# Performance work log

Hardware: AMD Instinct MI355X
Metric: run time of the kernel (lower is better)

The kernel has to match this reference:

```python
import jax, jax.numpy as jnp
import numpy as np

EPS = 1e-5  # torch BatchNorm1d default eps


def setup_inputs() -> dict:
    key = jax.random.key(0)
    ks = jax.random.split(key, 8)
    F, P = 32, 64            # frames, peds per frame
    B = F * P                # batch = 2048
    E, H, M, D = 64, 128, 512, 1024  # embed, h_dim, pool_mlp_dim, bottleneck
    starts = np.arange(F, dtype=np.int64) * P
    seq_start_end = jnp.asarray(np.stack([starts, starts + P], axis=1))
    inp = {
        "curr_h_states": jax.random.normal(ks[0], (1, B, H), dtype=jnp.float32),
        "curr_pos": jax.random.normal(ks[1], (B, 2), dtype=jnp.float32),
        "seq_start_end": seq_start_end,
        # embedding: Linear(2, E)
        "We": jax.random.normal(ks[2], (2, E), dtype=jnp.float32) * 0.5,
        "be": jnp.zeros((E,), dtype=jnp.float32),
        # mlp layer 1: Linear(E+H, M) + BN(M)
        "W1": jax.random.normal(ks[3], (E + H, M), dtype=jnp.float32) * 0.05,
        "b1": jnp.zeros((M,), dtype=jnp.float32),
        "g1": jnp.ones((M,), dtype=jnp.float32),
        "beta1": jnp.zeros((M,), dtype=jnp.float32),
        # mlp layer 2: Linear(M, D) + BN(D)
        "W2": jax.random.normal(ks[4], (M, D), dtype=jnp.float32) * 0.04,
        "b2": jnp.zeros((D,), dtype=jnp.float32),
        "g2": jnp.ones((D,), dtype=jnp.float32),
        "beta2": jnp.zeros((D,), dtype=jnp.float32),
        # BN running stats (eval mode)
        "rm1": jnp.zeros((M,), dtype=jnp.float32),
        "rv1": jnp.ones((M,), dtype=jnp.float32),
        "rm2": jnp.zeros((D,), dtype=jnp.float32),
        "rv2": jnp.ones((D,), dtype=jnp.float32),
    }
    return inp


def _bn(x, g, beta, rm, rv):
    return g * (x - rm) * jax.lax.rsqrt(rv + EPS) + beta


def reference(curr_h_states, curr_pos, seq_start_end, We, be, W1, b1, g1, beta1,
              W2, b2, g2, beta2, rm1, rv1, rm2, rv2):
    # Equal-size frames: vectorize the per-frame Python loop via a reshape.
    F = seq_start_end.shape[0]
    B = curr_h_states.shape[1]
    P = B // F
    h = curr_h_states[0].reshape(F, P, -1)      # (F, P, H)
    pos = curr_pos.reshape(F, P, 2)             # (F, P, 2)
    # rel_pos[f, i, j] = pos[f, j] - pos[f, i]  (repeat minus repeat_interleave)
    rel = pos[:, None, :, :] - pos[:, :, None, :]          # (F, P, P, 2)
    emb = rel @ We + be                                     # (F, P, P, E)
    h_rep = jnp.broadcast_to(h[:, None, :, :], (F, P, P, h.shape[-1]))
    x = jnp.concatenate([emb, h_rep], axis=-1)              # (F, P, P, E+H)
    x = jax.nn.relu(_bn(x @ W1 + b1, g1, beta1, rm1, rv1))  # (F, P, P, M)
    x = jax.nn.relu(_bn(x @ W2 + b2, g2, beta2, rm2, rv2))  # (F, P, P, D)
    pool_h = x.max(axis=2)                                  # max over j -> (F, P, D)
    return pool_h.reshape(B, -1)                            # (B, D)
```

## Files before the change

kernel.cpp:

```cpp
#include <hip/hip_runtime.h>
#include <hip/hip_fp16.h>
#include <stdint.h>

#define EPS_BN 1e-5f

constexpr int Fn = 32;
constexpr int Pn = 64;
constexpr int Bn = 2048;
constexpr int Hn = 128;
constexpr int En = 64;
constexpr int Mn = 512;
constexpr int Dn = 1024;

using f16x8   = __attribute__((ext_vector_type(8))) _Float16;
using f32x16  = __attribute__((ext_vector_type(16))) float;

static __device__ __forceinline__ unsigned short hfbits(float f) {
  return __builtin_bit_cast(unsigned short, __float2half(f));
}

static __device__ __forceinline__ void dma16(const uint4* g, const uint4* l) {
  __builtin_amdgcn_global_load_lds(
      (const __attribute__((address_space(1))) unsigned int*)g,
      (__attribute__((address_space(3))) unsigned int*)l, 16, 0, 0);
}

static __device__ __forceinline__ uint32_t pkmax(uint32_t a, uint32_t b) {
  uint32_t r;
  asm("v_pk_max_f16 %0, %1, %2" : "=v"(r) : "v"(a), "v"(b));
  return r;
}

static __device__ __forceinline__ void mk2(uint4 a0, uint4 a1, uint4 q,
                                           f16x8& r0, f16x8& r1) {
  uint4 x0, x1;
#pragma unroll
  for (int v = 0; v < 4; ++v) {
    uint32_t qw = ((const uint32_t*)&q)[v];
    ((uint32_t*)&x0)[v] = pkmax(((const uint32_t*)&a0)[v], qw);
    ((uint32_t*)&x1)[v] = pkmax(((const uint32_t*)&a1)[v], qw);
  }
  r0 = __builtin_bit_cast(f16x8, x0);
  r1 = __builtin_bit_cast(f16x8, x1);
}

__global__ void prep_all(const float* __restrict__ hs, const float* __restrict__ pos,
                         const float* __restrict__ We, const float* __restrict__ be,
                         const float* __restrict__ W1, const float* __restrict__ b1,
                         const float* __restrict__ g1, const float* __restrict__ beta1,
                         const float* __restrict__ rm1, const float* __restrict__ rv1,
                         const float* __restrict__ W2, const float* __restrict__ b2,
                         const float* __restrict__ g2, const float* __restrict__ beta2,
                         const float* __restrict__ rm2, const float* __restrict__ rv2,
                         __half* __restrict__ Agb, __half* __restrict__ Qgb,
                         uint4* __restrict__ W2g, float* __restrict__ G0,
                         float* __restrict__ G1, float* __restrict__ c2) {
  __shared__ float smem[64 * 65];
  int bid = blockIdx.x, t = threadIdx.x;
  if (bid < 512) {
    int rb = bid * 4, m = t;
    float w0 = 0.f, w1 = 0.f, c = 0.f;
    for (int e = 0; e < En; ++e) {
      float w = W1[e * Mn + m];
      w0 += We[e] * w; w1 += We[En + e] * w; c += be[e] * w;
    }
    c += b1[m];
    float s  = g1[m] * rsqrtf(rv1[m] + EPS_BN);
    float tt = beta1[m] - rm1[m] * s;
    float acc[4];
#pragma unroll
    for (int ri = 0; ri < 4; ++ri) acc[ri] = c;
#pragma unroll 4
    for (int e = 0; e < Hn; ++e) {
      float w = W1[(En + e) * Mn + m];
#pragma unroll
      for (int ri = 0; ri < 4; ++ri)
        acc[ri] += hs[(rb + ri) * Hn + e] * w;
    }
#pragma unroll
    for (int ri = 0; ri < 4; ++ri) {
      float q = pos[(rb + ri) * 2] * w0 + pos[(rb + ri) * 2 + 1] * w1;
      Agb[(rb + ri) * Mn + m] = __float2half((acc[ri] + q) * s + tt);
      Qgb[(rb + ri) * Mn + m] = __float2half(q * s);
    }
  } else if (bid < 640) {
    int b2i = bid - 512;
    int d0 = (b2i & 15) * 64, k0 = (b2i >> 4) * 64;
    int col = t & 63, row8 = t >> 6;
#pragma unroll
    for (int rr = 0; rr < 8; ++rr) {
      int row = rr * 8 + row8;
      smem[row * 65 + col] = W2[(k0 + row) * Dn + d0 + col];
    }
    __syncthreads();
    int lane = t & 63, q8 = t >> 6;
    int sel_n = q8 & 1, sel_ks = q8 >> 1;
    int dl = sel_n * 32 + (lane & 31), d = d0 + dl;
    float sf = g2[d] * rsqrtf(rv2[d] + EPS_BN);
    int kb = sel_ks * 16 + (lane >> 5) * 8;
    uint32_t wd[4];
#pragma unroll
    for (int h = 0; h < 4; ++h) {
      uint32_t u0 = hfbits(smem[(kb + 2 * h) * 65 + dl] * sf);
      uint32_t u1 = hfbits(smem[(kb + 2 * h + 1) * 65 + dl] * sf);
      wd[h] = u0 | (u1 << 16);
    }
    int n32 = (d0 >> 5) + sel_n;
    int ks  = (k0 >> 4) + sel_ks;
    W2g[(n32 * 32 + ks) * 64 + lane] = (uint4){wd[0], wd[1], wd[2], wd[3]};
  } else {
    int gb = bid - 640;
    int d0g = gb * 64;
    float* wr0 = smem;
    float* wr1 = smem + 512;
    {
      int m = t;
      float w0 = 0.f, w1 = 0.f;
      for (int e = 0; e < En; ++e) {
        float w = W1[e * Mn + m];
        w0 += We[e] * w; w1 += We[En + e] * w;
      }
      float s = g1[m] * rsqrtf(rv1[m] + EPS_BN);
      wr0[m] = w0 * s; wr1[m] = w1 * s;
    }
    __syncthreads();
    int dl = t & 63, part = t >> 6;
    float p0 = 0.f, p1 = 0.f;
#pragma unroll 4
    for (int mm = 0; mm < 64; ++mm) {
      int m = part * 64 + mm;
      float wv = W2[m * Dn + d0g + dl];
      p0 += wr0[m] * wv; p1 += wr1[m] * wv;
    }
    float* pr = smem + 1024;
    pr[part * 64 + dl] = p0;
    pr[512 + part * 64 + dl] = p1;
    __syncthreads();
    if (t < 128) {
      int which = t >> 6, dd = d0g + (t & 63);
      float s2v = g2[dd] * rsqrtf(rv2[dd] + EPS_BN);
      float sum = 0.f;
#pragma unroll
      for (int pp = 0; pp < 8; ++pp) sum += pr[which * 512 + pp * 64 + (t & 63)];
      (which ? G1 : G0)[dd] = sum * s2v;
      if (which == 0) c2[dd] = b2[dd] * s2v + beta2[dd] - rm2[dd] * s2v;
    }
  }
}

__launch_bounds__(256, 2)
__global__ void gemm_pool(const __half* __restrict__ Agb,
                          const __half* __restrict__ Qgb,
                          const uint4* __restrict__ W2g,
                          const float* __restrict__ pos,
                          const float* __restrict__ G0, const float* __restrict__ G1,
                          const float* __restrict__ c2, float* __restrict__ out) {
  __shared__ uint4 SH[3328];

  int wg  = blockIdx.x;
  int swz = (wg & 7) * 512 + (wg >> 3);
  int ct  = swz & 7;
  int rt  = swz >> 3;
  int f = rt >> 4, i0 = (rt & 15) * 4;

  int t = threadIdx.x, lane = t & 63, w = t >> 6;
  int i = i0 + w;

  const uint4* aGL = (const uint4*)(Agb + (size_t)f * Pn * Mn) +
                     (size_t)(lane & 31) * 64 + (lane >> 5);
  const uint4* bGL = W2g + (size_t)(4 * ct) * 32 * 64 + lane;

  auto stageAB = [&](int p) {
    int buf = p & 1;
    dma16(aGL + (size_t)0 * 2048 + (p * 4 + w) * 2, SH + buf * 512 + (w * 2 + 0) * 64);
    dma16(aGL + (size_t)1 * 2048 + (p * 4 + w) * 2, SH + buf * 512 + (w * 2 + 1) * 64);
#pragma unroll
    for (int nf = 0; nf < 4; ++nf)
      dma16(bGL + (nf * 32 + p * 4 + w) * 64,
            SH + 1024 + buf * 1024 + (w * 4 + nf) * 64);
  };

  dma16((const uint4*)(Qgb + (size_t)(f * Pn + i) * Mn) + lane, SH + 3072 + w * 64);
  stageAB(0);

  f32x16 acc[2][4];
#pragma unroll
  for (int jf = 0; jf < 2; ++jf)
#pragma unroll
    for (int nf = 0; nf < 4; ++nf)
      acc[jf][nf] = (f32x16){0.f,0.f,0.f,0.f,0.f,0.f,0.f,0.f,
                             0.f,0.f,0.f,0.f,0.f,0.f,0.f,0.f};

  int qb = 3072 + w * 64 + (lane >> 5);

#pragma unroll 1
  for (int p = 0; p < 8; ++p) {
    __syncthreads();
    if (p < 7) stageAB(p + 1);
    int ab = (p & 1) * 512 + lane;
    int bb = 1024 + (p & 1) * 1024 + lane;

#pragma unroll
    for (int ksl = 0; ksl < 4; ++ksl) {
      int ks = p * 4 + ksl;
      uint4 a0 = SH[ab + (ksl * 2 + 0) * 64];
      uint4 a1 = SH[ab + (ksl * 2 + 1) * 64];
      uint4 q  = SH[qb + ks * 2];
      f16x8 af0, af1;
      mk2(a0, a1, q, af0, af1);
#pragma unroll
      for (int nf = 0; nf < 4; ++nf) {
        f16x8 bg = __builtin_bit_cast(f16x8, SH[bb + (ksl * 4 + nf) * 64]);
        acc[0][nf] = __builtin_amdgcn_mfma_f32_32x32x16_f16(af0, bg, acc[0][nf], 0, 0, 0);
        acc[1][nf] = __builtin_amdgcn_mfma_f32_32x32x16_f16(af1, bg, acc[1][nf], 0, 0, 0);
      }
    }
  }

  float px = pos[(f * Pn + i) * 2], py = pos[(f * Pn + i) * 2 + 1];
#pragma unroll
  for (int nf = 0; nf < 4; ++nf) {
    float mx = -3.0e38f;
#pragma unroll
    for (int jf = 0; jf < 2; ++jf)
#pragma unroll
      for (int rg = 0; rg < 16; ++rg)
        mx = fmaxf(mx, acc[jf][nf][rg]);
    mx = fmaxf(mx, __shfl_xor(mx, 32));
    if (lane < 32) {
      int d = ct * 128 + nf * 32 + (lane & 31);
      float r = px * G0[d] + py * G1[d];
      out[(f * Pn + i) * Dn + d] = fmaxf(mx - r + c2[d], 0.f);
    }
  }
}

extern "C" void kernel_launch(void* const* d_in, const int* in_sizes, int n_in,
                              void* d_out, int out_size, void* d_ws, size_t ws_size,
                              hipStream_t stream) {
  const float* hs    = (const float*)d_in[0];
  const float* pos   = (const float*)d_in[1];
  const float* We    = (const float*)d_in[3];
  const float* be    = (const float*)d_in[4];
  const float* W1    = (const float*)d_in[5];
  const float* b1    = (const float*)d_in[6];
  const float* g1    = (const float*)d_in[7];
  const float* beta1 = (const float*)d_in[8];
  const float* W2    = (const float*)d_in[9];
  const float* b2    = (const float*)d_in[10];
  const float* g2    = (const float*)d_in[11];
  const float* beta2 = (const float*)d_in[12];
  const float* rm1   = (const float*)d_in[13];
  const float* rv1   = (const float*)d_in[14];
  const float* rm2   = (const float*)d_in[15];
  const float* rv2   = (const float*)d_in[16];

  char* ws = (char*)d_ws;
  float* c2 = (float*)(ws + 0);
  float* G0 = (float*)(ws + 4096);
  float* G1 = (float*)(ws + 8192);
  __half* Agb = (__half*)(ws + 12288);
  __half* Qgb = (__half*)(ws + 12288 + 2097152);
  uint4* W2g = (uint4*)(ws + 12288 + 2 * 2097152);
  float* out = (float*)d_out;

  prep_all<<<656, 512, 0, stream>>>(hs, pos, We, be, W1, b1, g1, beta1, rm1, rv1,
                                    W2, b2, g2, beta2, rm2, rv2, Agb, Qgb, W2g,
                                    G0, G1, c2);
  gemm_pool<<<4096, 256, 0, stream>>>(Agb, Qgb, W2g, pos, G0, G1, c2, out);
}
```

Baseline: 228.1 us.

## Compute two query rows per wave to reuse staged A/B tiles

Each wave now processes two pedestrian rows i instead of one, so one block covers eight rows and the grid is halved. The staged A and W2 tiles in shared memory are reused across both rows, roughly halving global and LDS traffic per MFMA. In exchange, accumulator registers double and launch bounds drop to one block per CU, reducing occupancy and latency hiding.

```diff
diff --git a/kernel.cpp b/kernel.cpp
--- a/kernel.cpp
+++ b/kernel.cpp
@@ -148,23 +148,23 @@
   }
 }
 
-__launch_bounds__(256, 2)
+__launch_bounds__(256, 1)
 __global__ void gemm_pool(const __half* __restrict__ Agb,
                           const __half* __restrict__ Qgb,
                           const uint4* __restrict__ W2g,
                           const float* __restrict__ pos,
                           const float* __restrict__ G0, const float* __restrict__ G1,
                           const float* __restrict__ c2, float* __restrict__ out) {
-  __shared__ uint4 SH[3328];
+  __shared__ uint4 SH[3584];
 
   int wg  = blockIdx.x;
-  int swz = (wg & 7) * 512 + (wg >> 3);
+  int swz = (wg & 7) * 256 + (wg >> 3);
   int ct  = swz & 7;
   int rt  = swz >> 3;
-  int f = rt >> 4, i0 = (rt & 15) * 4;
+  int f = rt >> 3, i0 = (rt & 7) * 8;
 
   int t = threadIdx.x, lane = t & 63, w = t >> 6;
-  int i = i0 + w;
+  int ia = i0 + w * 2, ib = ia + 1;
 
   const uint4* aGL = (const uint4*)(Agb + (size_t)f * Pn * Mn) +
                      (size_t)(lane & 31) * 64 + (lane >> 5);
@@ -180,18 +180,24 @@
             SH + 1024 + buf * 1024 + (w * 4 + nf) * 64);
   };
 
-  dma16((const uint4*)(Qgb + (size_t)(f * Pn + i) * Mn) + lane, SH + 3072 + w * 64);
+  dma16((const uint4*)(Qgb + (size_t)(f * Pn + ia) * Mn) + lane,
+        SH + 3072 + (w * 2 + 0) * 64);
+  dma16((const uint4*)(Qgb + (size_t)(f * Pn + ib) * Mn) + lane,
+        SH + 3072 + (w * 2 + 1) * 64);
   stageAB(0);
 
-  f32x16 acc[2][4];
-#pragma unroll
-  for (int jf = 0; jf < 2; ++jf)
-#pragma unroll
-    for (int nf = 0; nf < 4; ++nf)
-      acc[jf][nf] = (f32x16){0.f,0.f,0.f,0.f,0.f,0.f,0.f,0.f,
-                             0.f,0.f,0.f,0.f,0.f,0.f,0.f,0.f};
-
-  int qb = 3072 + w * 64 + (lane >> 5);
+  f32x16 acc[2][2][4];
+#pragma unroll
+  for (int ii = 0; ii < 2; ++ii)
+#pragma unroll
+    for (int jf = 0; jf < 2; ++jf)
+#pragma unroll
+      for (int nf = 0; nf < 4; ++nf)
+        acc[ii][jf][nf] = (f32x16){0.f,0.f,0.f,0.f,0.f,0.f,0.f,0.f,
+                                   0.f,0.f,0.f,0.f,0.f,0.f,0.f,0.f};
+
+  int qb0 = 3072 + (w * 2 + 0) * 64 + (lane >> 5);
+  int qb1 = 3072 + (w * 2 + 1) * 64 + (lane >> 5);
 
 #pragma unroll 1
   for (int p = 0; p < 8; ++p) {
@@ -205,32 +211,40 @@
       int ks = p * 4 + ksl;
       uint4 a0 = SH[ab + (ksl * 2 + 0) * 64];
       uint4 a1 = SH[ab + (ksl * 2 + 1) * 64];
-      uint4 q  = SH[qb + ks * 2];
-      f16x8 af0, af1;
-      mk2(a0, a1, q, af0, af1);
+      uint4 q0 = SH[qb0 + ks * 2];
+      uint4 q1 = SH[qb1 + ks * 2];
+      f16x8 af00, af01, af10, af11;
+      mk2(a0, a1, q0, af00, af01);
+      mk2(a0, a1, q1, af10, af11);
 #pragma unroll
       for (int nf = 0; nf < 4; ++nf) {
         f16x8 bg = __builtin_bit_cast(f16x8, SH[bb + (ksl * 4 + nf) * 64]);
-        acc[0][nf] = __builtin_amdgcn_mfma_f32_32x32x16_f16(af0, bg, acc[0][nf], 0, 0, 0);
-        acc[1][nf] = __builtin_amdgcn_mfma_f32_32x32x16_f16(af1, bg, acc[1][nf], 0, 0, 0);
+        acc[0][0][nf] = __builtin_amdgcn_mfma_f32_32x32x16_f16(af00, bg, acc[0][0][nf], 0, 0, 0);
+        acc[0][1][nf] = __builtin_amdgcn_mfma_f32_32x32x16_f16(af01, bg, acc[0][1][nf], 0, 0, 0);
+        acc[1][0][nf] = __builtin_amdgcn_mfma_f32_32x32x16_f16(af10, bg, acc[1][0][nf], 0, 0, 0);
+        acc[1][1][nf] = __builtin_amdgcn_mfma_f32_32x32x16_f16(af11, bg, acc[1][1][nf], 0, 0, 0);
       }
     }
   }
 
-  float px = pos[(f * Pn + i) * 2], py = pos[(f * Pn + i) * 2 + 1];
-#pragma unroll
-  for (int nf = 0; nf < 4; ++nf) {
-    float mx = -3.0e38f;
-#pragma unroll
-    for (int jf = 0; jf < 2; ++jf)
-#pragma unroll
-      for (int rg = 0; rg < 16; ++rg)
-        mx = fmaxf(mx, acc[jf][nf][rg]);
-    mx = fmaxf(mx, __shfl_xor(mx, 32));
-    if (lane < 32) {
-      int d = ct * 128 + nf * 32 + (lane & 31);
-      float r = px * G0[d] + py * G1[d];
-      out[(f * Pn + i) * Dn + d] = fmaxf(mx - r + c2[d], 0.f);
+#pragma unroll
+  for (int ii = 0; ii < 2; ++ii) {
+    int i = i0 + w * 2 + ii;
+    float px = pos[(f * Pn + i) * 2], py = pos[(f * Pn + i) * 2 + 1];
+#pragma unroll
+    for (int nf = 0; nf < 4; ++nf) {
+      float mx = -3.0e38f;
+#pragma unroll
+      for (int jf = 0; jf < 2; ++jf)
+#pragma unroll
+        for (int rg = 0; rg < 16; ++rg)
+          mx = fmaxf(mx, acc[ii][jf][nf][rg]);
+      mx = fmaxf(mx, __shfl_xor(mx, 32));
+      if (lane < 32) {
+        int d = ct * 128 + nf * 32 + (lane & 31);
+        float r = px * G0[d] + py * G1[d];
+        out[(f * Pn + i) * Dn + d] = fmaxf(mx - r + c2[d], 0.f);
+      }
     }
   }
 }
@@ -267,5 +281,5 @@
   prep_all<<<656, 512, 0, stream>>>(hs, pos, We, be, W1, b1, g1, beta1, rm1, rv1,
                                     W2, b2, g2, beta2, rm2, rv2, Agb, Qgb, W2g,
                                     G0, G1, c2);
-  gemm_pool<<<4096, 256, 0, stream>>>(Agb, Qgb, W2g, pos, G0, G1, c2, out);
-}
+  gemm_pool<<<2048, 256, 0, stream>>>(Agb, Qgb, W2g, pos, G0, G1, c2, out);
+}
```

After: 281.6 us. +23.5%, slower.
